# Performance work log

Measured on AMD Instinct MI355X. Metric: run time of the kernel, lower is better.

Reference implementation:

```python
import jax, jax.numpy as jnp
import numpy as np


def setup_inputs() -> dict:
    key = jax.random.key(0)
    ks = jax.random.split(key, 10)
    B, L, Din, Dout = 64, 512, 256, 256
    s = 0.05
    inp = jax.random.normal(ks[0], (B, L, Din), jnp.float32)
    ci = jax.random.randint(ks[1], (B, L), 0, L)
    # valid coref indices: ci[:, i] must be in [0, i] (refers to an already-produced state)
    ci = ci % (jnp.arange(L) + 1)[None, :]
    p = lambda k, sh: jax.random.normal(k, sh, jnp.float32) * s
    return {
        "inp": inp,
        "last_coref_idx": ci,
        "Wr": p(ks[2], (Din, Dout)), "br": jnp.zeros((Dout,), jnp.float32),
        "Ur": p(ks[3], (Dout, Dout)),
        "Wz": p(ks[4], (Din, Dout)), "bz": jnp.zeros((Dout,), jnp.float32),
        "Uz": p(ks[5], (Dout, Dout)),
        "Wh": p(ks[6], (Din, Dout)), "bh": jnp.zeros((Dout,), jnp.float32),
        "Uh": p(ks[7], (Dout, Dout)),
        "k1": p(ks[8], (Din, 1)),
        "k2": p(ks[9], (Din, 1)),
    }


def reference(inp, last_coref_idx, Wr, br, Ur, Wz, bz, Uz, Wh, bh, Uh, k1, k2):
    B, L, Din = inp.shape
    Dout = Wr.shape[1]
    split = Dout // 2
    bidx = jnp.arange(B)

    def step(carry, xs):
        h_last, hist = carry            # h_last [B,Dout], hist [L,B,Dout]
        x, c, i = xs                    # x [B,Din], c [B] int, i scalar step index
        # coref = state_history[c-1][b] if c > 0 else zeros
        coref = hist[jnp.clip(c - 1, 0), bidx]
        coref = jnp.where((c > 0)[:, None], coref, jnp.zeros_like(coref))
        # attention between h_last-half and coref-half
        e = jnp.concatenate([x @ k1, x @ k2], axis=1)      # [B,2]
        a = jax.nn.softmax(e, axis=1)[:, 0:1]              # [B,1]
        mt = jnp.concatenate([a * h_last[:, :split], (1.0 - a) * coref[:, split:]], axis=1)
        r = jax.nn.sigmoid(x @ Wr + br + mt @ Ur)
        z = jax.nn.sigmoid(x @ Wz + bz + mt @ Uz)
        h_ = jnp.tanh(x @ Wh + bh + r * (mt @ Uh))
        h = (1.0 - z) * mt + z * h_
        hist = jax.lax.dynamic_update_index_in_dim(hist, h, i, 0)
        return (h, hist), h

    h0 = jnp.zeros((B, Dout), inp.dtype)
    hist0 = jnp.zeros((L, B, Dout), inp.dtype)
    xs = (jnp.swapaxes(inp, 0, 1), jnp.swapaxes(last_coref_idx, 0, 1), jnp.arange(L))
    _, ys = jax.lax.scan(step, (h0, hist0), xs)            # ys [L,B,Dout]
    return jnp.swapaxes(ys, 0, 1)                          # [B,L,Dout]
```

## Files before the change

### kernel.cpp

```cpp
#include <hip/hip_runtime.h>
#include <stdint.h>
#include <stddef.h>

typedef _Float16 half_t;
typedef _Float16 half2_t __attribute__((ext_vector_type(2)));
typedef _Float16 half8_t __attribute__((ext_vector_type(8)));
typedef float    floatx4 __attribute__((ext_vector_type(4)));
typedef uint32_t u32x4   __attribute__((ext_vector_type(4)));
typedef int      intx4   __attribute__((ext_vector_type(4)));

#define SEQ_L 512
#define NBATCH 64
#define DIM 256
#define NTOT (NBATCH * SEQ_L)

__device__ __forceinline__ int dot4i8(uint32_t a, uint32_t b, int c) {
#if defined(__has_builtin)
#if __has_builtin(__builtin_amdgcn_sdot4)
  return __builtin_amdgcn_sdot4((int)a, (int)b, c, false);
#else
  int s = c;
  s += (int)(int8_t)(a)       * (int)(int8_t)(b);
  s += (int)(int8_t)(a >> 8)  * (int)(int8_t)(b >> 8);
  s += (int)(int8_t)(a >> 16) * (int)(int8_t)(b >> 16);
  s += (int)(int8_t)(a >> 24) * (int)(int8_t)(b >> 24);
  return s;
#endif
#else
  int s = c;
  s += (int)(int8_t)(a)       * (int)(int8_t)(b);
  s += (int)(int8_t)(a >> 8)  * (int)(int8_t)(b >> 8);
  s += (int)(int8_t)(a >> 16) * (int)(int8_t)(b >> 16);
  s += (int)(int8_t)(a >> 24) * (int)(int8_t)(b >> 24);
  return s;
#endif
}

__device__ __forceinline__ float sigmoidf_fast(float x) {
  return 1.0f / (1.0f + __expf(-x));
}
__device__ __forceinline__ float tanhf_fast(float x) {
  float e = __expf(2.0f * x);
  return 1.0f - 2.0f / (e + 1.0f);
}

__global__ void conv_w_kernel(const float* __restrict__ Wr,
                              const float* __restrict__ Wz,
                              const float* __restrict__ Wh,
                              half_t* __restrict__ Wt) {
  int n = blockIdx.x;
  int k = threadIdx.x;
  const float* W = (n < 256) ? Wr : ((n < 512) ? Wz : Wh);
  int j = n & 255;
  Wt[(size_t)n * DIM + k] = (half_t)W[(size_t)k * DIM + j];
}

__global__ __launch_bounds__(256) void attn_a_kernel(const float* __restrict__ inp,
                                                     const float* __restrict__ k1,
                                                     const float* __restrict__ k2,
                                                     float* __restrict__ a_arr) {
  int row  = blockIdx.x * 4 + (threadIdx.x >> 6);
  int lane = threadIdx.x & 63;
  const float4* x4 = (const float4*)(inp + (size_t)row * DIM);
  float4 xv  = x4[lane];
  float4 k1v = ((const float4*)k1)[lane];
  float4 k2v = ((const float4*)k2)[lane];
  float e1 = xv.x * k1v.x + xv.y * k1v.y + xv.z * k1v.z + xv.w * k1v.w;
  float e2 = xv.x * k2v.x + xv.y * k2v.y + xv.z * k2v.z + xv.w * k2v.w;
#pragma unroll
  for (int off = 32; off >= 1; off >>= 1) {
    e1 += __shfl_xor(e1, off);
    e2 += __shfl_xor(e2, off);
  }
  if (lane == 0) a_arr[row] = 1.0f / (1.0f + __expf(e2 - e1));
}

__global__ __launch_bounds__(256) void uscale_kernel(const float* __restrict__ Ur,
                                                     const float* __restrict__ Uz,
                                                     const float* __restrict__ Uh,
                                                     float* __restrict__ su) {
  const int g = blockIdx.x;
  const int j = threadIdx.x;
  const float* U = (g == 0) ? Ur : ((g == 1) ? Uz : Uh);
  float m = 0.0f;
  for (int k = 0; k < DIM; ++k) m = fmaxf(m, fabsf(U[(size_t)k * DIM + j]));
  su[g * DIM + j] = fmaxf(m, 1e-30f) * (1.0f / 127.0f);
}

__global__ __launch_bounds__(256) void upack_kernel(const float* __restrict__ Ur,
                                                    const float* __restrict__ Uz,
                                                    const float* __restrict__ Uh,
                                                    const float* __restrict__ su,
                                                    uint32_t* __restrict__ Ui8) {
  const int g = blockIdx.x;
  const int j = threadIdx.x;
  const float* U = (g == 0) ? Ur : ((g == 1) ? Uz : Uh);
  const float r = 1.0f / su[g * DIM + j];
  for (int q = 0; q < 64; ++q) {
    uint32_t w = 0;
#pragma unroll
    for (int t = 0; t < 4; ++t) {
      float v = U[(size_t)(q * 4 + t) * DIM + j] * r;
      int mi = __float2int_rn(v);
      mi = mi < -127 ? -127 : (mi > 127 ? 127 : mi);
      w |= ((uint32_t)(mi & 0xFF)) << (8 * t);
    }
    Ui8[((size_t)g * 64 + q) * DIM + j] = w;
  }
}

__global__ __launch_bounds__(256) void gemm_p_kernel(const float* __restrict__ X,
                                                     const half_t* __restrict__ Wt,
                                                     half_t* __restrict__ P) {
  __shared__ __align__(16) half_t As[128][32];
  __shared__ __align__(16) half_t Bs[128][32];
  const int tid  = threadIdx.x;
  const int bm   = blockIdx.x * 128;
  const int bn   = blockIdx.y * 128;
  const int lane = tid & 63;
  const int wave = tid >> 6;
  const int wm   = (wave >> 1) * 64;
  const int wn   = (wave & 1) * 64;
  const int quad = lane >> 4;
  const int l15  = lane & 15;
  const int r0   = tid >> 2;
  const int kc   = (tid & 3) * 8;

  floatx4 acc[4][4] = {};

  for (int k0 = 0; k0 < DIM; k0 += 32) {
#pragma unroll
    for (int hh = 0; hh < 2; ++hh) {
      int r = r0 + hh * 64;
      const float* asrc = X + (size_t)(bm + r) * DIM + k0 + kc;
      float4 f0 = *(const float4*)(asrc);
      float4 f1 = *(const float4*)(asrc + 4);
      half8_t av;
      av[0] = (half_t)f0.x; av[1] = (half_t)f0.y; av[2] = (half_t)f0.z; av[3] = (half_t)f0.w;
      av[4] = (half_t)f1.x; av[5] = (half_t)f1.y; av[6] = (half_t)f1.z; av[7] = (half_t)f1.w;
      *(half8_t*)(&As[r][kc]) = av;
      *(half8_t*)(&Bs[r][kc]) = *(const half8_t*)(Wt + (size_t)(bn + r) * DIM + k0 + kc);
    }
    __syncthreads();
    half8_t af[4], bf[4];
#pragma unroll
    for (int mi = 0; mi < 4; ++mi)
      af[mi] = *(const half8_t*)(&As[wm + mi * 16 + l15][quad * 8]);
#pragma unroll
    for (int ni = 0; ni < 4; ++ni)
      bf[ni] = *(const half8_t*)(&Bs[wn + ni * 16 + l15][quad * 8]);
#pragma unroll
    for (int mi = 0; mi < 4; ++mi)
#pragma unroll
      for (int ni = 0; ni < 4; ++ni)
        acc[mi][ni] = __builtin_amdgcn_mfma_f32_16x16x32_f16(af[mi], bf[ni], acc[mi][ni], 0, 0, 0);
    __syncthreads();
  }
#pragma unroll
  for (int mi = 0; mi < 4; ++mi)
#pragma unroll
    for (int ni = 0; ni < 4; ++ni) {
      int col = bn + wn + ni * 16 + l15;
#pragma unroll
      for (int rr = 0; rr < 4; ++rr) {
        int row = bm + wm + mi * 16 + quad * 4 + rr;
        P[(size_t)row * 768 + col] = (half_t)acc[mi][ni][rr];
      }
    }
}

__global__ __launch_bounds__(512, 1) void recur_kernel(
    const half_t* __restrict__ P,
    const float* __restrict__ a_arr,
    const int* __restrict__ cidx,
    const uint32_t* __restrict__ Ui8,
    const float* __restrict__ su,
    const float* __restrict__ br, const float* __restrict__ bz, const float* __restrict__ bh,
    float* __restrict__ out) {
  const int tid  = threadIdx.x;
  const int j    = tid & 255;
  const int half = tid >> 8;

  __shared__ __align__(16) half_t  hist[SEQ_L][128];
  __shared__ __align__(16) uint32_t mth8[64];
  __shared__ __align__(16) intx4  part[DIM];
  __shared__ __align__(16) float  ring[16][DIM];

  u32x4 ur8[8], uz8[8], uh8[8];
#pragma unroll
  for (int c8 = 0; c8 < 8; ++c8) {
#pragma unroll
    for (int t = 0; t < 4; ++t) {
      const int quad = half * 32 + c8 * 4 + t;
      ur8[c8][t] = Ui8[((size_t)0 * 64 + quad) * DIM + j];
      uz8[c8][t] = Ui8[((size_t)1 * 64 + quad) * DIM + j];
      uh8[c8][t] = Ui8[((size_t)2 * 64 + quad) * DIM + j];
    }
  }
  const float scr = su[0 * DIM + j] * (1.0f / 127.0f);
  const float scz = su[1 * DIM + j] * (1.0f / 127.0f);
  const float sch = su[2 * DIM + j] * (1.0f / 127.0f);
  const float brj = br[j], bzj = bz[j], bhj = bh[j];

  if (tid < 64) mth8[tid] = 0u;
  __syncthreads();

  float h   = 0.0f;
  float mtj = 0.0f;
  const int base = blockIdx.x * SEQ_L;

  float pr_c = 0.f, pz_c = 0.f, ph_c = 0.f;
  if (half == 0) {
    const half_t* prow = P + (size_t)base * 768;
    pr_c = (float)prow[j];
    pz_c = (float)prow[DIM + j];
    ph_c = (float)prow[2 * DIM + j];
  }
  float a_n = a_arr[base + 1];
  int   c_n = cidx[base + 1];

  for (int i = 0; i < SEQ_L; ++i) {
    float pr_x = 0.f, pz_x = 0.f, ph_x = 0.f;
    const int ip1 = (i + 1 < SEQ_L) ? (i + 1) : i;
    if (half == 0) {
      const half_t* prow = P + (size_t)(base + ip1) * 768;
      pr_x = (float)prow[j];
      pz_x = (float)prow[DIM + j];
      ph_x = (float)prow[2 * DIM + j];
    }
    const int ip2 = (i + 2 < SEQ_L) ? (i + 2) : (SEQ_L - 1);
    const float a_x = a_arr[base + ip2];
    const int   c_x = cidx[base + ip2];

    int ar = 0, az = 0, ah = 0;
    const u32x4* mq = (const u32x4*)(mth8 + half * 32);
#pragma unroll
    for (int c8 = 0; c8 < 8; ++c8) {
      u32x4 m4 = mq[c8];
      ar = dot4i8(m4.x, ur8[c8][0], ar);
      az = dot4i8(m4.x, uz8[c8][0], az);
      ah = dot4i8(m4.x, uh8[c8][0], ah);
      ar = dot4i8(m4.y, ur8[c8][1], ar);
      az = dot4i8(m4.y, uz8[c8][1], az);
      ah = dot4i8(m4.y, uh8[c8][1], ah);
      ar = dot4i8(m4.z, ur8[c8][2], ar);
      az = dot4i8(m4.z, uz8[c8][2], az);
      ah = dot4i8(m4.z, uh8[c8][2], ah);
      ar = dot4i8(m4.w, ur8[c8][3], ar);
      az = dot4i8(m4.w, uz8[c8][3], az);
      ah = dot4i8(m4.w, uh8[c8][3], ah);
    }
    if (half == 1) {
      intx4 p;
      p[0] = ar; p[1] = az; p[2] = ah; p[3] = 0;
      part[j] = p;
    }
    __syncthreads();

    if (half == 0) {
      intx4 p1 = part[j];
      const float fr = (float)(ar + p1[0]) * scr;
      const float fz = (float)(az + p1[1]) * scz;
      const float fh = (float)(ah + p1[2]) * sch;
      const float rg = sigmoidf_fast(pr_c + brj + fr);
      const float zg = sigmoidf_fast(pz_c + bzj + fz);
      const float hb = tanhf_fast(ph_c + bhj + rg * fh);
      h = (1.0f - zg) * mtj + zg * hb;
      ring[i & 15][j] = h;
      if (j >= 128) hist[i][j - 128] = (half_t)h;
      float mtn;
      if (j < 128) {
        mtn = a_n * h;
      } else {
        float coref = 0.0f;
        if (c_n > 0)
          coref = (c_n - 1 == i) ? h : (float)hist[c_n - 1][j - 128];
        mtn = (1.0f - a_n) * coref;
      }
      mtj = mtn;
      int mi = __float2int_rn(mtn * 127.0f);
      mi = mi < -127 ? -127 : (mi > 127 ? 127 : mi);
      unsigned v0 = (unsigned)mi & 0xFFu;
      unsigned v1 = (unsigned)__shfl_xor((int)v0, 1) & 0xFFu;
      unsigned pp = (j & 1) ? (v1 | (v0 << 8)) : (v0 | (v1 << 8));
      unsigned v2 = (unsigned)__shfl_xor((int)pp, 2);
      unsigned qd = (j & 2) ? ((v2 & 0xFFFFu) | (pp << 16))
                            : ((pp & 0xFFFFu) | (v2 << 16));
      if ((j & 3) == 0) mth8[j >> 2] = qd;
    } else {
      if ((i & 7) == 0 && i > 0) {
#pragma unroll
        for (int rr = 0; rr < 8; ++rr) {
          const int row = i - 8 + rr;
          out[(size_t)(base + row) * DIM + j] = ring[row & 15][j];
        }
      }
    }
    pr_c = pr_x; pz_c = pz_x; ph_c = ph_x;
    a_n = a_x;   c_n = c_x;
    __syncthreads();
  }

#pragma unroll
  for (int rr = 0; rr < 4; ++rr) {
    const int idx = rr * 512 + tid;
    const int row = 504 + (idx >> 8);
    const int col = idx & 255;
    out[(size_t)(base + row) * DIM + col] = ring[row & 15][col];
  }
}

extern "C" void kernel_launch(void* const* d_in, const int* in_sizes, int n_in,
                              void* d_out, int out_size, void* d_ws, size_t ws_size,
                              hipStream_t stream) {
  const float* inp = (const float*)d_in[0];
  const int*   ci  = (const int*)d_in[1];
  const float* Wr  = (const float*)d_in[2];
  const float* br  = (const float*)d_in[3];
  const float* Ur  = (const float*)d_in[4];
  const float* Wz  = (const float*)d_in[5];
  const float* bz  = (const float*)d_in[6];
  const float* Uz  = (const float*)d_in[7];
  const float* Wh  = (const float*)d_in[8];
  const float* bh  = (const float*)d_in[9];
  const float* Uh  = (const float*)d_in[10];
  const float* k1  = (const float*)d_in[11];
  const float* k2  = (const float*)d_in[12];
  float* out = (float*)d_out;

  char* ws = (char*)d_ws;
  half_t*   Wt    = (half_t*)ws;
  half_t*   P     = (half_t*)(ws + 393216);
  float*    a_arr = (float*)(ws + 393216 + 50331648);
  float*    su    = (float*)(ws + 50855936);
  uint32_t* Ui8   = (uint32_t*)(ws + 50859008);

  conv_w_kernel<<<dim3(768), dim3(256), 0, stream>>>(Wr, Wz, Wh, Wt);
  attn_a_kernel<<<dim3(NTOT / 4), dim3(256), 0, stream>>>(inp, k1, k2, a_arr);
  uscale_kernel<<<dim3(3), dim3(256), 0, stream>>>(Ur, Uz, Uh, su);
  upack_kernel<<<dim3(3), dim3(256), 0, stream>>>(Ur, Uz, Uh, su, Ui8);
  gemm_p_kernel<<<dim3(NTOT / 128, 6), dim3(256), 0, stream>>>(inp, Wt, P);
  recur_kernel<<<dim3(NBATCH), dim3(512), 0, stream>>>(P, a_arr, ci, Ui8, su,
                                                       br, bz, bh, out);
}
```

Baseline: 737.6 us.

## Interleave K-split across lane pairs and double-buffer mt to drop a barrier

Each output column j is now handled by two adjacent lanes, each holding half the K range, instead of two separate 256-thread halves. The partial dot products are combined with a cross-lane shuffle rather than through shared memory plus an extra __syncthreads, and the quantized mt vector is double-buffered so one barrier per step is enough. Both lanes redundantly compute the gate nonlinearities, and output is written directly each step instead of through a staging ring. Launch bounds are raised to 2 blocks per CU, which adds register pressure on the int8 weight registers.

```diff
diff --git a/kernel.cpp b/kernel.cpp
--- a/kernel.cpp
+++ b/kernel.cpp
@@ -169,7 +169,7 @@
     }
 }
 
-__global__ __launch_bounds__(512, 1) void recur_kernel(
+__global__ __launch_bounds__(512, 2) void recur_kernel(
     const half_t* __restrict__ P,
     const float* __restrict__ a_arr,
     const int* __restrict__ cidx,
@@ -178,13 +178,11 @@
     const float* __restrict__ br, const float* __restrict__ bz, const float* __restrict__ bh,
     float* __restrict__ out) {
   const int tid  = threadIdx.x;
-  const int j    = tid & 255;
-  const int half = tid >> 8;
-
-  __shared__ __align__(16) half_t  hist[SEQ_L][128];
-  __shared__ __align__(16) uint32_t mth8[64];
-  __shared__ __align__(16) intx4  part[DIM];
-  __shared__ __align__(16) float  ring[16][DIM];
+  const int j    = tid >> 1;
+  const int half = tid & 1;
+
+  __shared__ __align__(16) half_t   hist[SEQ_L][128];
+  __shared__ __align__(16) uint32_t mtb[2][64];
 
   u32x4 ur8[8], uz8[8], uh8[8];
 #pragma unroll
@@ -197,43 +195,49 @@
       uh8[c8][t] = Ui8[((size_t)2 * 64 + quad) * DIM + j];
     }
   }
+#pragma unroll
+  for (int c8 = 0; c8 < 8; ++c8) {
+    asm volatile("" : "+v"(ur8[c8]), "+v"(uz8[c8]), "+v"(uh8[c8]));
+  }
+
   const float scr = su[0 * DIM + j] * (1.0f / 127.0f);
   const float scz = su[1 * DIM + j] * (1.0f / 127.0f);
   const float sch = su[2 * DIM + j] * (1.0f / 127.0f);
   const float brj = br[j], bzj = bz[j], bhj = bh[j];
 
-  if (tid < 64) mth8[tid] = 0u;
-  __syncthreads();
-
-  float h   = 0.0f;
+  if (tid < 64) mtb[0][tid] = 0u;
+
   float mtj = 0.0f;
   const int base = blockIdx.x * SEQ_L;
 
-  float pr_c = 0.f, pz_c = 0.f, ph_c = 0.f;
-  if (half == 0) {
-    const half_t* prow = P + (size_t)base * 768;
-    pr_c = (float)prow[j];
-    pz_c = (float)prow[DIM + j];
-    ph_c = (float)prow[2 * DIM + j];
-  }
+  const half_t* prow0 = P + (size_t)base * 768;
+  float pr_c = (float)prow0[j];
+  float pz_c = (float)prow0[DIM + j];
+  float ph_c = (float)prow0[2 * DIM + j];
   float a_n = a_arr[base + 1];
   int   c_n = cidx[base + 1];
 
+  __syncthreads();
+
   for (int i = 0; i < SEQ_L; ++i) {
-    float pr_x = 0.f, pz_x = 0.f, ph_x = 0.f;
     const int ip1 = (i + 1 < SEQ_L) ? (i + 1) : i;
-    if (half == 0) {
-      const half_t* prow = P + (size_t)(base + ip1) * 768;
-      pr_x = (float)prow[j];
-      pz_x = (float)prow[DIM + j];
-      ph_x = (float)prow[2 * DIM + j];
-    }
+    const half_t* prow = P + (size_t)(base + ip1) * 768;
+    float pr_x = (float)prow[j];
+    float pz_x = (float)prow[DIM + j];
+    float ph_x = (float)prow[2 * DIM + j];
     const int ip2 = (i + 2 < SEQ_L) ? (i + 2) : (SEQ_L - 1);
     const float a_x = a_arr[base + ip2];
     const int   c_x = cidx[base + ip2];
 
+    const int  cp    = c_n - 1;
+    const bool use_h = (cp == i);
+    float corefv = 0.0f;
+    if (j >= 128) {
+      if (c_n > 0 && !use_h) corefv = (float)hist[cp][j - 128];
+    }
+
     int ar = 0, az = 0, ah = 0;
-    const u32x4* mq = (const u32x4*)(mth8 + half * 32);
+    const u32x4* mq = (const u32x4*)(&mtb[i & 1][half * 32]);
 #pragma unroll
     for (int c8 = 0; c8 < 8; ++c8) {
       u32x4 m4 = mq[c8];
@@ -250,63 +254,46 @@
       az = dot4i8(m4.w, uz8[c8][3], az);
       ah = dot4i8(m4.w, uh8[c8][3], ah);
     }
-    if (half == 1) {
-      intx4 p;
-      p[0] = ar; p[1] = az; p[2] = ah; p[3] = 0;
-      part[j] = p;
-    }
-    __syncthreads();
-
-    if (half == 0) {
-      intx4 p1 = part[j];
-      const float fr = (float)(ar + p1[0]) * scr;
-      const float fz = (float)(az + p1[1]) * scz;
-      const float fh = (float)(ah + p1[2]) * sch;
-      const float rg = sigmoidf_fast(pr_c + brj + fr);
-      const float zg = sigmoidf_fast(pz_c + bzj + fz);
-      const float hb = tanhf_fast(ph_c + bhj + rg * fh);
-      h = (1.0f - zg) * mtj + zg * hb;
-      ring[i & 15][j] = h;
+    ar += __shfl_xor(ar, 1);
+    az += __shfl_xor(az, 1);
+    ah += __shfl_xor(ah, 1);
+
+    const float fr = (float)ar * scr;
+    const float fz = (float)az * scz;
+    const float fh = (float)ah * sch;
+    const float rg = sigmoidf_fast(pr_c + brj + fr);
+    const float zg = sigmoidf_fast(pz_c + bzj + fz);
+    const float hb = tanhf_fast(ph_c + bhj + rg * fh);
+    const float h  = (1.0f - zg) * mtj + zg * hb;
+
+    if (tid & 1) {
+      out[(size_t)(base + i) * DIM + j] = h;
       if (j >= 128) hist[i][j - 128] = (half_t)h;
-      float mtn;
-      if (j < 128) {
-        mtn = a_n * h;
-      } else {
-        float coref = 0.0f;
-        if (c_n > 0)
-          coref = (c_n - 1 == i) ? h : (float)hist[c_n - 1][j - 128];
-        mtn = (1.0f - a_n) * coref;
-      }
-      mtj = mtn;
-      int mi = __float2int_rn(mtn * 127.0f);
-      mi = mi < -127 ? -127 : (mi > 127 ? 127 : mi);
-      unsigned v0 = (unsigned)mi & 0xFFu;
-      unsigned v1 = (unsigned)__shfl_xor((int)v0, 1) & 0xFFu;
-      unsigned pp = (j & 1) ? (v1 | (v0 << 8)) : (v0 | (v1 << 8));
-      unsigned v2 = (unsigned)__shfl_xor((int)pp, 2);
-      unsigned qd = (j & 2) ? ((v2 & 0xFFFFu) | (pp << 16))
-                            : ((pp & 0xFFFFu) | (v2 << 16));
-      if ((j & 3) == 0) mth8[j >> 2] = qd;
+    }
+
+    float mtn;
+    if (j < 128) {
+      mtn = a_n * h;
     } else {
-      if ((i & 7) == 0 && i > 0) {
-#pragma unroll
-        for (int rr = 0; rr < 8; ++rr) {
-          const int row = i - 8 + rr;
-          out[(size_t)(base + row) * DIM + j] = ring[row & 15][j];
-        }
-      }
-    }
+      const float coref = (c_n > 0) ? (use_h ? h : corefv) : 0.0f;
+      mtn = (1.0f - a_n) * coref;
+    }
+    mtj = mtn;
+
+    int mi = __float2int_rn(mtn * 127.0f);
+    mi = mi < -127 ? -127 : (mi > 127 ? 127 : mi);
+    unsigned v0 = (unsigned)mi & 0xFFu;
+    unsigned o1 = (unsigned)__shfl_xor((int)v0, 2) & 0xFFu;
+    unsigned pp = (j & 1) ? (o1 | (v0 << 8)) : (v0 | (o1 << 8));
+    unsigned o2 = (unsigned)__shfl_xor((int)pp, 4);
+    unsigned qd = (j & 2) ? ((o2 & 0xFFFFu) | (pp << 16))
+                          : ((pp & 0xFFFFu) | (o2 << 16));
+    if ((tid & 7) == 0) mtb[(i + 1) & 1][j >> 2] = qd;
+
     pr_c = pr_x; pz_c = pz_x; ph_c = ph_x;
     a_n = a_x;   c_n = c_x;
+
     __syncthreads();
-  }
-
-#pragma unroll
-  for (int rr = 0; rr < 4; ++rr) {
-    const int idx = rr * 512 + tid;
-    const int row = 504 + (idx >> 8);
-    const int col = idx & 255;
-    out[(size_t)(base + row) * DIM + col] = ring[row & 15][col];
   }
 }
 
```

Result: slower. 753.6 us (+2.2%).
